# Kernel tuning notes

Measured on AMD Instinct MI355X. Metric: run time of the kernel, lower is better.

## Reference

```python
import jax, jax.numpy as jnp
import numpy as np

B, T, I, H, L = 64, 128, 4096, 1024, 2


def _xavier(key, shape):
    fan_in, fan_out = shape[-1], shape[-2]
    limit = np.sqrt(6.0 / (fan_in + fan_out)).astype(np.float32)
    return jax.random.uniform(key, shape, jnp.float32, -limit, limit)


def setup_inputs() -> dict:
    key = jax.random.key(0)
    ks = jax.random.split(key, 8)
    x = jax.random.normal(ks[0], (B, T, I), jnp.float32)
    h0 = jnp.zeros((L, B, H), jnp.float32)
    c0 = jnp.zeros((L, B, H), jnp.float32)
    # layer 0: input dim I; layer 1: input dim H. Gates stacked [i, f, c, o]; peephole V stacked [i, f, o].
    Wx0 = _xavier(ks[1], (4, H, I))
    Uh0 = _xavier(ks[2], (4, H, H))
    Vc0 = _xavier(ks[3], (3, H, H))
    b0 = jnp.zeros((4, H), jnp.float32)
    Wx1 = _xavier(ks[4], (4, H, H))
    Uh1 = _xavier(ks[5], (4, H, H))
    Vc1 = _xavier(ks[6], (3, H, H))
    b1 = jnp.zeros((4, H), jnp.float32)
    return {"x": x, "h0": h0, "c0": c0,
            "Wx0": Wx0, "Uh0": Uh0, "Vc0": Vc0, "b0": b0,
            "Wx1": Wx1, "Uh1": Uh1, "Vc1": Vc1, "b1": b1}


def _cell(x_t, h, c, Wx, Uh, Vc, b):
    # x_t: (B, D_in); h, c: (B, H). Peephole LSTM (o-gate peeps at OLD c, as in source).
    xz = jnp.einsum('bi,ghi->gbh', x_t, Wx)          # (4, B, H)
    hz = jnp.einsum('bh,gkh->gbk', h, Uh)            # (4, B, H)
    cz = jnp.einsum('bh,gkh->gbk', c, Vc)            # (3, B, H) for [i, f, o]
    i = jax.nn.sigmoid(xz[0] + hz[0] + cz[0] + b[0])
    f = jax.nn.sigmoid(xz[1] + hz[1] + cz[1] + b[1])
    g = jnp.tanh(xz[2] + hz[2] + b[2])
    new_c = f * c + i * g
    o = jax.nn.sigmoid(xz[3] + hz[3] + cz[2] + b[3])
    new_h = o * jnp.tanh(new_c)
    return new_h, new_c


def reference(x, h0, c0, Wx0, Uh0, Vc0, b0, Wx1, Uh1, Vc1, b1):
    def step(carry, x_t):
        ha, ca, hb, cb = carry
        ha, ca = _cell(x_t, ha, ca, Wx0, Uh0, Vc0, b0)
        hb, cb = _cell(ha, hb, cb, Wx1, Uh1, Vc1, b1)
        return (ha, ca, hb, cb), hb

    init = (h0[0], c0[0], h0[1], c0[1])
    (ha, ca, hb, cb), out = jax.lax.scan(step, init, jnp.swapaxes(x, 0, 1))
    output = jnp.swapaxes(out, 0, 1)                 # (B, T, H)
    h_n = jnp.stack([ha, hb], axis=0)                # (L, B, H)
    c_n = jnp.stack([ca, cb], axis=0)
    return output, h_n, c_n
```

## Files before the change

### kernel.cpp

```cpp
#include <hip/hip_runtime.h>
#include <math.h>

#define BB 64
#define TT 128
#define II 4096
#define HH 1024
#define NG 4096
#define K0 2048
#define K1 3072

typedef __attribute__((ext_vector_type(8))) short short8;
typedef __attribute__((ext_vector_type(4))) float f32x4;
typedef __attribute__((ext_vector_type(4))) unsigned short ushort4v;
typedef __attribute__((ext_vector_type(8))) unsigned short ushort8v;

__device__ __forceinline__ unsigned short f2bf(float f){
  union { float f; unsigned u; } v; v.f = f;
  unsigned r = v.u + 0x7fffu + ((v.u >> 16) & 1u);
  return (unsigned short)(r >> 16);
}
__device__ __forceinline__ float bf2f(unsigned short u){
  union { float f; unsigned u; } v; v.u = ((unsigned)u) << 16;
  return v.f;
}
__device__ __forceinline__ float sigm(float x){ return 1.f/(1.f + expf(-x)); }

__device__ __forceinline__ int fidx(int bb, int k){
  return (((k >> 5)*4 + (bb >> 4))*64 + ((bb & 15) | (((k >> 3) & 3) << 4)))*8 + (k & 7);
}


__global__ void conv_x(const float* __restrict__ in, unsigned short* __restrict__ outb){
  const size_t i = ((size_t)blockIdx.x*256 + threadIdx.x)*4;
  f32x4 v = *(const f32x4*)(&in[i]);
  ushort4v o; o[0]=f2bf(v[0]); o[1]=f2bf(v[1]); o[2]=f2bf(v[2]); o[3]=f2bf(v[3]);
  *(ushort4v*)(&outb[i]) = o;
}

__global__ void build_Wx0il(const float* __restrict__ Wx0, unsigned short* __restrict__ Wil){
  const int row = blockIdx.y;
  const int c4 = (blockIdx.x*256 + threadIdx.x)*4;
  const int g = row & 3, h = row >> 2;
  f32x4 v = *(const f32x4*)(&Wx0[((size_t)(g*HH + h))*II + c4]);
  ushort4v o; o[0]=f2bf(v[0]); o[1]=f2bf(v[1]); o[2]=f2bf(v[2]); o[3]=f2bf(v[3]);
  *(ushort4v*)(&Wil[(size_t)row*II + c4]) = o;
}

__global__ void build_W0f(const float* __restrict__ Uh0, const float* __restrict__ Vc0,
                          unsigned short* __restrict__ Wf){
  const int n0 = blockIdx.y*16, kb = blockIdx.x*128;
  const int nr = threadIdx.x & 15, kc = threadIdx.x >> 4;
  const int n = n0 + nr, k8 = kb + kc*8;
  const int g = n & 3, hid = n >> 2;
  float v[8];
  if (k8 < HH){
    const float* src = &Uh0[((size_t)(g*HH+hid))*HH + k8];
    #pragma unroll
    for (int e=0;e<8;e++) v[e]=src[e];
  } else if (g == 2){
    #pragma unroll
    for (int e=0;e<8;e++) v[e]=0.f;
  } else {
    const int jj = (g==3)?2:g;
    const float* src = &Vc0[((size_t)(jj*HH+hid))*HH + (k8-HH)];
    #pragma unroll
    for (int e=0;e<8;e++) v[e]=src[e];
  }
  ushort8v o;
  #pragma unroll
  for (int e=0;e<8;e++) o[e]=f2bf(v[e]);
  const int chunk = (n>>4)*(K0/32) + (k8>>5);
  const int lanew = nr | (((k8>>3)&3)<<4);
  *(ushort8v*)(&Wf[((size_t)chunk*64 + lanew)*8]) = o;
}

__global__ void build_W1f(const float* __restrict__ Wx1, const float* __restrict__ Uh1,
                          const float* __restrict__ Vc1, unsigned short* __restrict__ Wf){
  const int n0 = blockIdx.y*16, kb = blockIdx.x*128;
  const int nr = threadIdx.x & 15, kc = threadIdx.x >> 4;
  const int n = n0 + nr, k8 = kb + kc*8;
  const int g = n & 3, hid = n >> 2;
  float v[8];
  if (k8 < HH){
    const float* src = &Wx1[((size_t)(g*HH+hid))*HH + k8];
    #pragma unroll
    for (int e=0;e<8;e++) v[e]=src[e];
  } else if (k8 < 2*HH){
    const float* src = &Uh1[((size_t)(g*HH+hid))*HH + (k8-HH)];
    #pragma unroll
    for (int e=0;e<8;e++) v[e]=src[e];
  } else if (g == 2){
    #pragma unroll
    for (int e=0;e<8;e++) v[e]=0.f;
  } else {
    const int jj = (g==3)?2:g;
    const float* src = &Vc1[((size_t)(jj*HH+hid))*HH + (k8-2*HH)];
    #pragma unroll
    for (int e=0;e<8;e++) v[e]=src[e];
  }
  ushort8v o;
  #pragma unroll
  for (int e=0;e<8;e++) o[e]=f2bf(v[e]);
  const int chunk = (n>>4)*(K1/32) + (k8>>5);
  const int lanew = nr | (((k8>>3)&3)<<4);
  *(ushort8v*)(&Wf[((size_t)chunk*64 + lanew)*8]) = o;
}

__global__ void init_state2(const float* __restrict__ h0, const float* __restrict__ c0,
  float* __restrict__ ca_f, float* __restrict__ cb_f,
  unsigned short* __restrict__ A0w, unsigned short* __restrict__ A1w){
  const int idx = blockIdx.x*256 + threadIdx.x;
  const int b = idx >> 10, k = idx & 1023;
  const float ha = h0[idx], ca = c0[idx];
  const float hb = h0[BB*HH + idx], cb = c0[BB*HH + idx];
  ca_f[idx]=ca; cb_f[idx]=cb;
  A0w[fidx(b, k)]        = f2bf(ha);
  A0w[fidx(b, HH + k)]   = f2bf(ca);
  A1w[fidx(b, HH + k)]   = f2bf(hb);
  A1w[fidx(b, 2*HH + k)] = f2bf(cb);
}

__global__ __launch_bounds__(256) void gemm_xz0(
  const unsigned short* __restrict__ A, const unsigned short* __restrict__ Wt,
  const float* __restrict__ b0, unsigned short* __restrict__ C)
{
  __shared__ __align__(16) unsigned short Asm[128*72];
  __shared__ __align__(16) unsigned short Wsm[128*72];
  const int tid = threadIdx.x, lane = tid & 63, w = tid >> 6;
  const int wr = w >> 1, wc = w & 1;
  const int m0 = blockIdx.y * 128, n0 = blockIdx.x * 128;
  const int rA = tid >> 3, c8 = (tid & 7) * 8;

  f32x4 acc[4][4];
  #pragma unroll
  for (int i=0;i<4;i++)
    #pragma unroll
    for (int j=0;j<4;j++) acc[i][j] = f32x4{0.f,0.f,0.f,0.f};

  ushort8v pa[4], pw[4];
  #pragma unroll
  for (int s=0;s<4;s++){
    pa[s] = *(const ushort8v*)(&A [(size_t)(m0 + rA + 32*s)*II + c8]);
    pw[s] = *(const ushort8v*)(&Wt[(size_t)(n0 + rA + 32*s)*II + c8]);
  }
  for (int kt = 0; kt < II; kt += 64) {
    __syncthreads();
    #pragma unroll
    for (int s=0;s<4;s++){
      *(ushort8v*)(&Asm[(rA+32*s)*72 + c8]) = pa[s];
      *(ushort8v*)(&Wsm[(rA+32*s)*72 + c8]) = pw[s];
    }
    __syncthreads();
    if (kt + 64 < II){
      #pragma unroll
      for (int s=0;s<4;s++){
        pa[s] = *(const ushort8v*)(&A [(size_t)(m0 + rA + 32*s)*II + kt + 64 + c8]);
        pw[s] = *(const ushort8v*)(&Wt[(size_t)(n0 + rA + 32*s)*II + kt + 64 + c8]);
      }
    }
    #pragma unroll
    for (int ks=0; ks<2; ks++){
      const int kk = ks*32 + (lane>>4)*8;
      short8 af[4], bfv[4];
      #pragma unroll
      for (int rt=0; rt<4; rt++)
        af[rt] = *(const short8*)(&Asm[(wr*64 + rt*16 + (lane&15))*72 + kk]);
      #pragma unroll
      for (int ct=0; ct<4; ct++)
        bfv[ct] = *(const short8*)(&Wsm[(wc*64 + ct*16 + (lane&15))*72 + kk]);
      #pragma unroll
      for (int rt=0; rt<4; rt++)
        #pragma unroll
        for (int ct=0; ct<4; ct++)
          acc[rt][ct] = __builtin_amdgcn_mfma_f32_16x16x32_bf16(af[rt], bfv[ct], acc[rt][ct], 0,0,0);
    }
  }
  #pragma unroll
  for (int rt=0; rt<4; rt++){
    #pragma unroll
    for (int ct=0; ct<4; ct++){
      const int n = n0 + wc*64 + ct*16 + (lane&15);
      const float bias = b0[(n&3)*HH + (n>>2)];
      #pragma unroll
      for (int r=0;r<4;r++){
        const int m = m0 + wr*64 + rt*16 + (lane>>4)*4 + r;
        const int row = (m & 127)*BB + (m >> 7);
        C[(size_t)row*NG + n] = f2bf(acc[rt][ct][r] + bias);
      }
    }
  }
}


template<int NJ>
__device__ __forceinline__ void gemm_frag_w(const unsigned short* __restrict__ Af,
                                            const unsigned short* __restrict__ Wfb,
                                            int wave, int lane, f32x4 (&acc)[4])
{
  const unsigned short* abase = Af  + ((size_t)(wave*NJ*4)*64 + lane)*8;
  const unsigned short* wbase = Wfb + ((size_t)(wave*NJ)*64 + lane)*8;
  short8 wf[NJ];
  #pragma unroll
  for (int j = 0; j < NJ; ++j)
    wf[j] = *(const short8*)(wbase + (size_t)(j*64)*8);
  short8 buf[4][4];
  #pragma unroll
  for (int j = 0; j < NJ + 3; ++j) {
    if (j < NJ) {
      #pragma unroll
      for (int m = 0; m < 4; ++m)
        buf[j & 3][m] = *(const short8*)(abase + (size_t)((j*4 + m)*64)*8);
    }
    if (j >= 3) {
      const int jc = j - 3;
      #pragma unroll
      for (int m = 0; m < 4; ++m)
        acc[m] = __builtin_amdgcn_mfma_f32_16x16x32_bf16(buf[jc & 3][m], wf[jc], acc[m], 0, 0, 0);
    }
  }
}

__global__ __launch_bounds__(256, 2) void lstm_step_fused(
  const unsigned short* __restrict__ A0r, unsigned short* __restrict__ A0n,
  const unsigned short* __restrict__ A1r, unsigned short* __restrict__ A1w,
  const unsigned short* __restrict__ W0f, const unsigned short* __restrict__ W1f,
  const unsigned short* __restrict__ XZ0, const float* __restrict__ b1v,
  float* __restrict__ ca_f, float* __restrict__ cb_f,
  float* __restrict__ out, int t)
{
  __shared__ float preSm[4][64][17];
  const int tid = threadIdx.x, lane = tid & 63, wave = tid >> 6;
  const int bb = tid >> 2, kl = tid & 3;
  float* outp = out + (size_t)BB*TT*HH;

  if (blockIdx.x < 256) {
    if (t >= TT) return;
    const int blk = blockIdx.x, n0 = blk*16, kh = blk*4 + kl;
    f32x4 acc[4];
    #pragma unroll
    for (int m=0;m<4;m++) acc[m] = f32x4{0.f,0.f,0.f,0.f};
    gemm_frag_w<16>(A0r, W0f + (size_t)blk*(K0/32)*64*8, wave, lane, acc);
    #pragma unroll
    for (int m=0;m<4;m++)
      #pragma unroll
      for (int r=0;r<4;r++)
        preSm[wave][m*16 + (lane>>4)*4 + r][lane & 15] = acc[m][r];
    __syncthreads();
    float p0=0.f,p1=0.f,p2=0.f,p3=0.f;
    #pragma unroll
    for (int w2=0; w2<4; ++w2){
      p0 += preSm[w2][bb][4*kl+0];
      p1 += preSm[w2][bb][4*kl+1];
      p2 += preSm[w2][bb][4*kl+2];
      p3 += preSm[w2][bb][4*kl+3];
    }
    ushort4v xz = *(const ushort4v*)(&XZ0[((size_t)t*BB + bb)*NG + n0 + 4*kl]);
    p0 += bf2f(xz[0]); p1 += bf2f(xz[1]); p2 += bf2f(xz[2]); p3 += bf2f(xz[3]);
    const float ig = sigm(p0), fg = sigm(p1), gg = tanhf(p2), og = sigm(p3);
    const int si = bb*HH + kh;
    const float cn = fg*ca_f[si] + ig*gg;
    const float hn = og*tanhf(cn);
    ca_f[si] = cn;
    const unsigned short h16 = f2bf(hn), c16 = f2bf(cn);
    A0n[fidx(bb, kh)]      = h16;
    A0n[fidx(bb, HH + kh)] = c16;
    A1w[fidx(bb, kh)]      = h16;
    if (t == TT-1){ outp[si] = hn; outp[2*BB*HH + si] = cn; }
  } else {
    if (t == 0) return;
    const int blk = blockIdx.x - 256, n0 = blk*16, kh = blk*4 + kl;
    const int tb = t - 1;
    f32x4 acc[4];
    #pragma unroll
    for (int m=0;m<4;m++) acc[m] = f32x4{0.f,0.f,0.f,0.f};
    gemm_frag_w<24>(A1r, W1f + (size_t)blk*(K1/32)*64*8, wave, lane, acc);
    #pragma unroll
    for (int m=0;m<4;m++)
      #pragma unroll
      for (int r=0;r<4;r++)
        preSm[wave][m*16 + (lane>>4)*4 + r][lane & 15] = acc[m][r];
    __syncthreads();
    float p0 = b1v[kh], p1 = b1v[HH+kh], p2 = b1v[2*HH+kh], p3 = b1v[3*HH+kh];
    #pragma unroll
    for (int w2=0; w2<4; ++w2){
      p0 += preSm[w2][bb][4*kl+0];
      p1 += preSm[w2][bb][4*kl+1];
      p2 += preSm[w2][bb][4*kl+2];
      p3 += preSm[w2][bb][4*kl+3];
    }
    const float ig = sigm(p0), fg = sigm(p1), gg = tanhf(p2), og = sigm(p3);
    const int si = bb*HH + kh;
    const float cn = fg*cb_f[si] + ig*gg;
    const float hn = og*tanhf(cn);
    cb_f[si] = cn;
    A1w[fidx(bb, HH + kh)]   = f2bf(hn);
    A1w[fidx(bb, 2*HH + kh)] = f2bf(cn);
    out[((size_t)bb*TT + tb)*HH + kh] = hn;
    if (tb == TT-1){ outp[BB*HH + si] = hn; outp[3*BB*HH + si] = cn; }
  }
}


extern "C" void kernel_launch(void* const* d_in, const int* in_sizes, int n_in,
                              void* d_out, int out_size, void* d_ws, size_t ws_size,
                              hipStream_t stream)
{
  (void)in_sizes; (void)n_in; (void)out_size; (void)ws_size;
  const float* x   = (const float*)d_in[0];
  const float* h0  = (const float*)d_in[1];
  const float* c0  = (const float*)d_in[2];
  const float* Wx0 = (const float*)d_in[3];
  const float* Uh0 = (const float*)d_in[4];
  const float* Vc0 = (const float*)d_in[5];
  const float* b0  = (const float*)d_in[6];
  const float* Wx1 = (const float*)d_in[7];
  const float* Uh1 = (const float*)d_in[8];
  const float* Vc1 = (const float*)d_in[9];
  const float* b1  = (const float*)d_in[10];
  float* out = (float*)d_out;

  char* ws = (char*)d_ws;
  size_t off = 0;
  auto alloc = [&](size_t bytes) { char* p = ws + off; off += (bytes + 255) & ~(size_t)255; return p; };
  unsigned short* x_bf  = (unsigned short*)alloc((size_t)BB*TT*II*2);
  unsigned short* Wx0il = (unsigned short*)alloc((size_t)NG*II*2);
  unsigned short* XZ0   = (unsigned short*)alloc((size_t)BB*TT*NG*2);
  unsigned short* W0f   = (unsigned short*)alloc((size_t)NG*K0*2);
  unsigned short* W1f   = (unsigned short*)alloc((size_t)NG*K1*2);
  unsigned short* A0b[2] = { (unsigned short*)alloc((size_t)BB*K0*2), (unsigned short*)alloc((size_t)BB*K0*2) };
  unsigned short* A1b[2] = { (unsigned short*)alloc((size_t)BB*K1*2), (unsigned short*)alloc((size_t)BB*K1*2) };
  float* ca_f = (float*)alloc((size_t)BB*HH*4);
  float* cb_f = (float*)alloc((size_t)BB*HH*4);

  conv_x<<<32768, 256, 0, stream>>>(x, x_bf);
  build_Wx0il<<<dim3(4,4096), 256, 0, stream>>>(Wx0, Wx0il);
  build_W0f<<<dim3(K0/128, NG/16), 256, 0, stream>>>(Uh0, Vc0, W0f);
  build_W1f<<<dim3(K1/128, NG/16), 256, 0, stream>>>(Wx1, Uh1, Vc1, W1f);
  init_state2<<<256, 256, 0, stream>>>(h0, c0, ca_f, cb_f, A0b[0], A1b[0]);
  gemm_xz0<<<dim3(32,64), 256, 0, stream>>>(x_bf, Wx0il, b0, XZ0);

  for (int t = 0; t <= TT; ++t) {
    const int q = t & 1;
    lstm_step_fused<<<512, 256, 0, stream>>>(
        A0b[q], A0b[q^1],
        A1b[q^1], A1b[q],
        W0f, W1f, XZ0, b1, ca_f, cb_f, out, t);
  }
}
```

Before: 2.405 ms.

## Widen per-block gate tile to 32 columns, halving step-kernel blocks

```diff
diff --git a/kernel.cpp b/kernel.cpp
--- a/kernel.cpp
+++ b/kernel.cpp
@@ -192,17 +192,21 @@
 }
 
 
-template<int NJ>
-__device__ __forceinline__ void gemm_frag_w(const unsigned short* __restrict__ Af,
-                                            const unsigned short* __restrict__ Wfb,
-                                            int wave, int lane, f32x4 (&acc)[4])
+template<int KC>
+__device__ __forceinline__ void gemm_frag32(const unsigned short* __restrict__ Af,
+                                            const unsigned short* __restrict__ Wfull,
+                                            int cg0, int wave, int lane, f32x4 (&acc)[4][2])
 {
-  const unsigned short* abase = Af  + ((size_t)(wave*NJ*4)*64 + lane)*8;
-  const unsigned short* wbase = Wfb + ((size_t)(wave*NJ)*64 + lane)*8;
-  short8 wf[NJ];
-  #pragma unroll
-  for (int j = 0; j < NJ; ++j)
-    wf[j] = *(const short8*)(wbase + (size_t)(j*64)*8);
+  constexpr int NJ = KC/4;
+  const unsigned short* abase = Af + ((size_t)(wave*NJ*4)*64 + lane)*8;
+  const unsigned short* wb0 = Wfull + ((size_t)((cg0+0)*KC + wave*NJ)*64 + lane)*8;
+  const unsigned short* wb1 = Wfull + ((size_t)((cg0+1)*KC + wave*NJ)*64 + lane)*8;
+  short8 wf[NJ][2];
+  #pragma unroll
+  for (int j = 0; j < NJ; ++j){
+    wf[j][0] = *(const short8*)(wb0 + (size_t)(j*64)*8);
+    wf[j][1] = *(const short8*)(wb1 + (size_t)(j*64)*8);
+  }
   short8 buf[4][4];
   #pragma unroll
   for (int j = 0; j < NJ + 3; ++j) {
@@ -214,13 +218,15 @@
     if (j >= 3) {
       const int jc = j - 3;
       #pragma unroll
-      for (int m = 0; m < 4; ++m)
-        acc[m] = __builtin_amdgcn_mfma_f32_16x16x32_bf16(buf[jc & 3][m], wf[jc], acc[m], 0, 0, 0);
-    }
-  }
-}
-
-__global__ __launch_bounds__(256, 2) void lstm_step_fused(
+      for (int m = 0; m < 4; ++m){
+        acc[m][0] = __builtin_amdgcn_mfma_f32_16x16x32_bf16(buf[jc & 3][m], wf[jc][0], acc[m][0], 0, 0, 0);
+        acc[m][1] = __builtin_amdgcn_mfma_f32_16x16x32_bf16(buf[jc & 3][m], wf[jc][1], acc[m][1], 0, 0, 0);
+      }
+    }
+  }
+}
+
+__global__ __launch_bounds__(256, 1) void lstm_step_fused(
   const unsigned short* __restrict__ A0r, unsigned short* __restrict__ A0n,
   const unsigned short* __restrict__ A1r, unsigned short* __restrict__ A1w,
   const unsigned short* __restrict__ W0f, const unsigned short* __restrict__ W1f,
@@ -228,75 +234,90 @@
   float* __restrict__ ca_f, float* __restrict__ cb_f,
   float* __restrict__ out, int t)
 {
-  __shared__ float preSm[4][64][17];
+  __shared__ float preSm[4][64][33];
   const int tid = threadIdx.x, lane = tid & 63, wave = tid >> 6;
-  const int bb = tid >> 2, kl = tid & 3;
   float* outp = out + (size_t)BB*TT*HH;
 
-  if (blockIdx.x < 256) {
+  if (blockIdx.x < 128) {
     if (t >= TT) return;
-    const int blk = blockIdx.x, n0 = blk*16, kh = blk*4 + kl;
-    f32x4 acc[4];
-    #pragma unroll
-    for (int m=0;m<4;m++) acc[m] = f32x4{0.f,0.f,0.f,0.f};
-    gemm_frag_w<16>(A0r, W0f + (size_t)blk*(K0/32)*64*8, wave, lane, acc);
+    const int blk = blockIdx.x, n0 = blk*32;
+    f32x4 acc[4][2];
+    #pragma unroll
+    for (int m=0;m<4;m++){ acc[m][0] = f32x4{0.f,0.f,0.f,0.f}; acc[m][1] = f32x4{0.f,0.f,0.f,0.f}; }
+    gemm_frag32<K0/32>(A0r, W0f, blk*2, wave, lane, acc);
     #pragma unroll
     for (int m=0;m<4;m++)
       #pragma unroll
-      for (int r=0;r<4;r++)
-        preSm[wave][m*16 + (lane>>4)*4 + r][lane & 15] = acc[m][r];
+      for (int c=0;c<2;c++)
+        #pragma unroll
+        for (int r=0;r<4;r++)
+          preSm[wave][m*16 + (lane>>4)*4 + r][c*16 + (lane & 15)] = acc[m][c][r];
     __syncthreads();
-    float p0=0.f,p1=0.f,p2=0.f,p3=0.f;
-    #pragma unroll
-    for (int w2=0; w2<4; ++w2){
-      p0 += preSm[w2][bb][4*kl+0];
-      p1 += preSm[w2][bb][4*kl+1];
-      p2 += preSm[w2][bb][4*kl+2];
-      p3 += preSm[w2][bb][4*kl+3];
-    }
-    ushort4v xz = *(const ushort4v*)(&XZ0[((size_t)t*BB + bb)*NG + n0 + 4*kl]);
-    p0 += bf2f(xz[0]); p1 += bf2f(xz[1]); p2 += bf2f(xz[2]); p3 += bf2f(xz[3]);
-    const float ig = sigm(p0), fg = sigm(p1), gg = tanhf(p2), og = sigm(p3);
-    const int si = bb*HH + kh;
-    const float cn = fg*ca_f[si] + ig*gg;
-    const float hn = og*tanhf(cn);
-    ca_f[si] = cn;
-    const unsigned short h16 = f2bf(hn), c16 = f2bf(cn);
-    A0n[fidx(bb, kh)]      = h16;
-    A0n[fidx(bb, HH + kh)] = c16;
-    A1w[fidx(bb, kh)]      = h16;
-    if (t == TT-1){ outp[si] = hn; outp[2*BB*HH + si] = cn; }
+    #pragma unroll
+    for (int e=0;e<2;++e){
+      const int idx = tid + e*256;
+      const int b = idx >> 3, kl = idx & 7;
+      const int kh = blk*8 + kl;
+      float p0=0.f,p1=0.f,p2=0.f,p3=0.f;
+      #pragma unroll
+      for (int w2=0; w2<4; ++w2){
+        p0 += preSm[w2][b][4*kl+0];
+        p1 += preSm[w2][b][4*kl+1];
+        p2 += preSm[w2][b][4*kl+2];
+        p3 += preSm[w2][b][4*kl+3];
+      }
+      ushort4v xz = *(const ushort4v*)(&XZ0[((size_t)t*BB + b)*NG + n0 + 4*kl]);
+      p0 += bf2f(xz[0]); p1 += bf2f(xz[1]); p2 += bf2f(xz[2]); p3 += bf2f(xz[3]);
+      const float ig = sigm(p0), fg = sigm(p1), gg = tanhf(p2), og = sigm(p3);
+      const int si = b*HH + kh;
+      const float cn = fg*ca_f[si] + ig*gg;
+      const float hn = og*tanhf(cn);
+      ca_f[si] = cn;
+      const unsigned short h16 = f2bf(hn), c16 = f2bf(cn);
+      A0n[fidx(b, kh)]      = h16;
+      A0n[fidx(b, HH + kh)] = c16;
+      A1w[fidx(b, kh)]      = h16;
+      if (t == TT-1){ outp[si] = hn; outp[2*BB*HH + si] = cn; }
+    }
   } else {
     if (t == 0) return;
-    const int blk = blockIdx.x - 256, n0 = blk*16, kh = blk*4 + kl;
+    const int blk = blockIdx.x - 128, n0 = blk*32;
     const int tb = t - 1;
-    f32x4 acc[4];
-    #pragma unroll
-    for (int m=0;m<4;m++) acc[m] = f32x4{0.f,0.f,0.f,0.f};
-    gemm_frag_w<24>(A1r, W1f + (size_t)blk*(K1/32)*64*8, wave, lane, acc);
+    f32x4 acc[4][2];
+    #pragma unroll
+    for (int m=0;m<4;m++){ acc[m][0] = f32x4{0.f,0.f,0.f,0.f}; acc[m][1] = f32x4{0.f,0.f,0.f,0.f}; }
+    gemm_frag32<K1/32>(A1r, W1f, blk*2, wave, lane, acc);
     #pragma unroll
     for (int m=0;m<4;m++)
       #pragma unroll
-      for (int r=0;r<4;r++)
-        preSm[wave][m*16 + (lane>>4)*4 + r][lane & 15] = acc[m][r];
+      for (int c=0;c<2;c++)
+        #pragma unroll
+        for (int r=0;r<4;r++)
+          preSm[wave][m*16 + (lane>>4)*4 + r][c*16 + (lane & 15)] = acc[m][c][r];
     __syncthreads();
-    float p0 = b1v[kh], p1 = b1v[HH+kh], p2 = b1v[2*HH+kh], p3 = b1v[3*HH+kh];
-    #pragma unroll
-    for (int w2=0; w2<4; ++w2){
-      p0 += preSm[w2][bb][4*kl+0];
-      p1 += preSm[w2][bb][4*kl+1];
-      p2 += preSm[w2][bb][4*kl+2];
-      p3 += preSm[w2][bb][4*kl+3];
-    }
-    const float ig = sigm(p0), fg = sigm(p1), gg = tanhf(p2), og = sigm(p3);
-    const int si = bb*HH + kh;
-    const float cn = fg*cb_f[si] + ig*gg;
-    const float hn = og*tanhf(cn);
-    cb_f[si] = cn;
-    A1w[fidx(bb, HH + kh)]   = f2bf(hn);
-    A1w[fidx(bb, 2*HH + kh)] = f2bf(cn);
-    out[((size_t)bb*TT + tb)*HH + kh] = hn;
-    if (tb == TT-1){ outp[BB*HH + si] = hn; outp[3*BB*HH + si] = cn; }
+    #pragma unroll
+    for (int e=0;e<2;++e){
+      const int idx = tid + e*256;
+      const int b = idx >> 3, kl = idx & 7;
+      const int kh = blk*8 + kl;
+      float p0 = b1v[kh], p1 = b1v[HH+kh], p2 = b1v[2*HH+kh], p3 = b1v[3*HH+kh];
+      #pragma unroll
+      for (int w2=0; w2<4; ++w2){
+        p0 += preSm[w2][b][4*kl+0];
+        p1 += preSm[w2][b][4*kl+1];
+        p2 += preSm[w2][b][4*kl+2];
+        p3 += preSm[w2][b][4*kl+3];
+      }
+      const float ig = sigm(p0), fg = sigm(p1), gg = tanhf(p2), og = sigm(p3);
+      const int si = b*HH + kh;
+      const float cn = fg*cb_f[si] + ig*gg;
+      const float hn = og*tanhf(cn);
+      cb_f[si] = cn;
+      A1w[fidx(b, HH + kh)]   = f2bf(hn);
+      A1w[fidx(b, 2*HH + kh)] = f2bf(cn);
+      out[((size_t)b*TT + tb)*HH + kh] = hn;
+      if (tb == TT-1){ outp[BB*HH + si] = hn; outp[3*BB*HH + si] = cn; }
+    }
   }
 }
 
@@ -341,7 +362,7 @@
 
   for (int t = 0; t <= TT; ++t) {
     const int q = t & 1;
-    lstm_step_fused<<<512, 256, 0, stream>>>(
+    lstm_step_fused<<<256, 256, 0, stream>>>(
         A0b[q], A0b[q^1],
         A1b[q^1], A1b[q],
         W0f, W1f, XZ0, b1, ca_f, cb_f, out, t);
```

Measured after the change: 2.806 ms. 1.17x slower.
